# Kernel optimization log

Hardware: AMD Instinct MI355X
Metric: run time of the kernel (lower is better)

## Reference

```python
import jax, jax.numpy as jnp
import numpy as np

LN_EPS = 1e-5

def _layer_norm(x, g, b):
    mu = jnp.mean(x, axis=-1, keepdims=True)
    var = jnp.mean(jnp.square(x - mu), axis=-1, keepdims=True)
    return (x - mu) * jax.lax.rsqrt(var + LN_EPS) * g + b

def setup_inputs() -> dict:
    key = jax.random.key(0)
    ks = jax.random.split(key, 12)
    B, L, E, H, W = 4, 1024, 1024, 16, 128
    s = 0.02
    return {
        "x": jax.random.normal(ks[0], (B, L, E), dtype=jnp.float32),
        "in_proj_w": jax.random.normal(ks[1], (3 * E, E), dtype=jnp.float32) * s,
        "in_proj_b": jnp.zeros((3 * E,), dtype=jnp.float32),
        "out_proj_w": jax.random.normal(ks[2], (E, E), dtype=jnp.float32) * s,
        "out_proj_b": jnp.zeros((E,), dtype=jnp.float32),
        "ln1_g": jnp.ones((E,), dtype=jnp.float32),
        "ln1_b": jnp.zeros((E,), dtype=jnp.float32),
        "w1": jax.random.normal(ks[3], (4 * E, E), dtype=jnp.float32) * s,
        "b1": jnp.zeros((4 * E,), dtype=jnp.float32),
        "w2": jax.random.normal(ks[4], (E, 4 * E), dtype=jnp.float32) * s,
        "b2": jnp.zeros((E,), dtype=jnp.float32),
        "ln2_g": jnp.ones((E,), dtype=jnp.float32),
        "ln2_b": jnp.zeros((E,), dtype=jnp.float32),
        "n_head": 16,
        "window_size": 128,
    }

def reference(x, in_proj_w, in_proj_b, out_proj_w, out_proj_b,
              ln1_g, ln1_b, w1, b1, w2, b2, ln2_g, ln2_b,
              n_head, window_size):
    B, L, E = x.shape
    H = n_head
    D = E // H
    # qkv projection (torch Linear convention: y = x @ W.T + b)
    qkv = jnp.einsum('ble,fe->blf', x, in_proj_w) + in_proj_b  # [B,L,3E]
    q, k, v = jnp.split(qkv, 3, axis=-1)
    q = q.reshape(B, L, H, D).transpose(0, 2, 1, 3)  # [B,H,L,D]
    k = k.reshape(B, L, H, D).transpose(0, 2, 1, 3)
    v = v.reshape(B, L, H, D).transpose(0, 2, 1, 3)
    scores = jnp.einsum('bhld,bhmd->bhlm', q, k) / np.sqrt(D)  # [B,H,L,L]
    # banded window mask: allowed iff |i-j| <= window_size (same as the double loop)
    idx = jnp.arange(L)
    band = jnp.abs(idx[:, None] - idx[None, :]) <= window_size  # [L,L]
    scores = jnp.where(band[None, None], scores, -jnp.inf)
    attn = jax.nn.softmax(scores, axis=-1)  # [B,H,L,L]
    ctx = jnp.einsum('bhlm,bhmd->bhld', attn, v)  # [B,H,L,D]
    ctx = ctx.transpose(0, 2, 1, 3).reshape(B, L, E)
    attn_out = jnp.einsum('ble,fe->blf', ctx, out_proj_w) + out_proj_b
    attn_weights = jnp.mean(attn, axis=1)  # torch MHA averages heads -> [B,L,L]
    # residual + norm1 (dropout is identity in eval)
    h = _layer_norm(x + attn_out, ln1_g, ln1_b)
    # positionwise FFN
    ff = jnp.einsum('ble,fe->blf', h, w1) + b1
    ff = jax.nn.relu(ff)
    ff = jnp.einsum('blf,ef->ble', ff, w2) + b2
    out = _layer_norm(h + ff, ln2_g, ln2_b)
    return (out, attn_weights)
```

## Files before the change

kernel.cpp:

```cpp
#include <hip/hip_runtime.h>

#define BB 4
#define LL 1024
#define EE 1024
#define HH 16
#define DD 64

typedef __attribute__((ext_vector_type(8))) short short8;
typedef __attribute__((ext_vector_type(4))) float floatx4;

#define PSTR ((size_t)4096 * 1024)

__device__ __forceinline__ float bf2f(short s) {
    union { unsigned u; float f; } c;
    c.u = ((unsigned)(unsigned short)s) << 16;
    return c.f;
}
__device__ __forceinline__ short f2bf(float f) {
    union { float f; unsigned u; } c; c.f = f;
    unsigned r = c.u + 0x7fffu + ((c.u >> 16) & 1u);
    return (short)(r >> 16);
}

__device__ __forceinline__ void async_copy16(const void* g, void* l) {
    __builtin_amdgcn_global_load_lds(
        (const __attribute__((address_space(1))) unsigned int*)g,
        (__attribute__((address_space(3))) unsigned int*)l, 16, 0, 0);
}

__global__ __launch_bounds__(256) void cvt5(
    const float* __restrict__ x, const float* __restrict__ wqkv,
    const float* __restrict__ wo, const float* __restrict__ w1,
    const float* __restrict__ w2,
    short* __restrict__ xb, short* __restrict__ wqkvb, short* __restrict__ wob,
    short* __restrict__ w1b, short* __restrict__ w2b)
{
    int bi = blockIdx.x;
    const float* in; short* out; int base;
    if      (bi <  4096) { in = x;    out = xb;    base = 0;     }
    else if (bi <  7168) { in = wqkv; out = wqkvb; base = 4096;  }
    else if (bi <  8192) { in = wo;   out = wob;   base = 7168;  }
    else if (bi < 12288) { in = w1;   out = w1b;   base = 8192;  }
    else                 { in = w2;   out = w2b;   base = 12288; }
    int i = (bi - base) * 256 + threadIdx.x;
    float4 v = ((const float4*)in)[i];
    unsigned long long u =
          (unsigned long long)(unsigned short)f2bf(v.x)
        | ((unsigned long long)(unsigned short)f2bf(v.y) << 16)
        | ((unsigned long long)(unsigned short)f2bf(v.z) << 32)
        | ((unsigned long long)(unsigned short)f2bf(v.w) << 48);
    ((unsigned long long*)out)[i] = u;
}

template<bool RELU, bool SK, bool WVT>
__global__ __launch_bounds__(512, 2) void gemm256(
    const short* __restrict__ A, const short* __restrict__ Bw,
    const float* __restrict__ bias,
    short* __restrict__ Cb, short* __restrict__ VTp,
    int M, int N, int K, int Ksp)
{
    __shared__ short SH[67584];
    const int tid  = threadIdx.x;
    const int w    = tid >> 6, lane = tid & 63;
    const int fr   = lane & 15, quad = lane >> 4;
    const int wm   = w >> 2,  wn   = w & 3;

    const int gx   = gridDim.x;
    const int flat = blockIdx.y * gx + blockIdx.x;
    const int nwg  = gx * gridDim.y;
    const int q8   = nwg >> 3;
    const int swz  = (flat & 7) * q8 + (flat >> 3);
    const int m0   = (swz % gx) * 256;
    const int n0   = (swz / gx) * 256;

    const int kb = SK ? blockIdx.z * Ksp : 0;
    const int NT = (SK ? Ksp : K) >> 6;

    const int srow = w * 8 + (lane >> 3);
    const int sg   = lane & 7;
    auto stage = [&](int s) {
        if (s >= NT) return;
#pragma unroll
        for (int i = 0; i < 4; ++i) {
            int r = i * 64 + srow;
            int g = sg ^ (r & 7);
            async_copy16(A + (size_t)(m0 + r) * K + kb + s * 64 + g * 8,
                         SH + (s & 1) * 32768 + i * 4096 + w * 512);
        }
#pragma unroll
        for (int i = 0; i < 4; ++i) {
            int r = i * 64 + srow;
            int g = sg ^ (r & 7);
            async_copy16(Bw + (size_t)(n0 + r) * K + kb + s * 64 + g * 8,
                         SH + (s & 1) * 32768 + 16384 + i * 4096 + w * 512);
        }
    };

    floatx4 acc[8][4];
#pragma unroll
    for (int i = 0; i < 8; ++i)
#pragma unroll
        for (int j = 0; j < 4; ++j) acc[i][j] = (floatx4){0.f, 0.f, 0.f, 0.f};

    stage(0);

    const int posk0 = ((quad    ) ^ (fr & 7)) * 8;
    const int posk1 = ((4 + quad) ^ (fr & 7)) * 8;

    for (int t = 0; t < NT; ++t) {
        __syncthreads();
        __builtin_amdgcn_sched_barrier(0);

        const short* sA = SH + (t & 1) * 32768;
        const short* sB = sA + 16384;

        stage(t + 1);

        short8 a0[8], b0[4];
#pragma unroll
        for (int i = 0; i < 8; ++i) a0[i] = *(const short8*)&sA[(wm * 128 + i * 16 + fr) * 64 + posk0];
#pragma unroll
        for (int j = 0; j < 4; ++j) b0[j] = *(const short8*)&sB[(wn * 64 + j * 16 + fr) * 64 + posk0];
        __builtin_amdgcn_s_setprio(1);
#pragma unroll
        for (int i = 0; i < 8; ++i)
#pragma unroll
            for (int j = 0; j < 4; ++j)
                acc[i][j] = __builtin_amdgcn_mfma_f32_16x16x32_bf16(a0[i], b0[j], acc[i][j], 0, 0, 0);
        __builtin_amdgcn_s_setprio(0);

        short8 a1[8], b1[4];
#pragma unroll
        for (int i = 0; i < 8; ++i) a1[i] = *(const short8*)&sA[(wm * 128 + i * 16 + fr) * 64 + posk1];
#pragma unroll
        for (int j = 0; j < 4; ++j) b1[j] = *(const short8*)&sB[(wn * 64 + j * 16 + fr) * 64 + posk1];
        __builtin_amdgcn_s_setprio(1);
#pragma unroll
        for (int i = 0; i < 8; ++i)
#pragma unroll
            for (int j = 0; j < 4; ++j)
                acc[i][j] = __builtin_amdgcn_mfma_f32_16x16x32_bf16(a1[i], b1[j], acc[i][j], 0, 0, 0);
        __builtin_amdgcn_s_setprio(0);
    }

    __syncthreads();

    const int cc = lane & 15, rb4 = quad * 4;
    const bool vblk = WVT && (n0 >= 2048);

    if (!vblk) {
#pragma unroll
        for (int i = 0; i < 8; ++i) {
            int row = wm * 128 + i * 16 + rb4;
#pragma unroll
            for (int j = 0; j < 4; ++j) {
                int col = wn * 64 + j * 16 + cc;
                float bv = SK ? 0.0f : bias[n0 + col];
#pragma unroll
                for (int r = 0; r < 4; ++r) {
                    float v = acc[i][j][r] + bv;
                    if (RELU) v = fmaxf(v, 0.0f);
                    SH[(row + r) * 264 + col] = f2bf(v);
                }
            }
        }
    } else {
#pragma unroll
        for (int i = 0; i < 8; ++i) {
            int row = wm * 128 + i * 16 + rb4;
#pragma unroll
            for (int j = 0; j < 4; ++j) {
                int col = wn * 64 + j * 16 + cc;
                float bv = bias[n0 + col];
#pragma unroll
                for (int r = 0; r < 4; ++r)
                    SH[col * 264 + row + r] = f2bf(acc[i][j][r] + bv);
            }
        }
    }
    __syncthreads();

    if (!vblk) {
        short* Co = Cb + (SK ? (size_t)blockIdx.z * PSTR : 0);
#pragma unroll
        for (int it = 0; it < 16; ++it) {
            int idx = it * 512 + tid;
            int row = idx >> 5, ch = idx & 31;
            short8 v = *(const short8*)&SH[row * 264 + ch * 8];
            *(short8*)&Co[(size_t)(m0 + row) * N + n0 + ch * 8] = v;
        }
    } else {
        const int bI = m0 >> 10, m0l = m0 & 1023;
#pragma unroll
        for (int it = 0; it < 16; ++it) {
            int idx = it * 512 + tid;
            int col = idx >> 5, tc = idx & 31;
            int gc  = n0 + col - 2048;
            int h   = gc >> 6, d = gc & 63;
            short8 v = *(const short8*)&SH[col * 264 + tc * 8];
            *(short8*)&VTp[((size_t)((bI * 16 + h) * 64 + d)) * 1024 + m0l + tc * 8] = v;
        }
    }
}

template<bool RELU, bool SK>
__global__ __launch_bounds__(256) void gemm_bt(
    const short* __restrict__ A, const short* __restrict__ Bw,
    const float* __restrict__ bias,
    short* __restrict__ Cb,
    int M, int N, int K, int Ksp)
{
    __shared__ union U {
        struct { short As[128 * 64]; short Bs[128 * 64]; } s;
        short Cs[128 * 136];
    } u;
    const int tid  = threadIdx.x;
    const int wave = tid >> 6, lane = tid & 63;
    const int m0 = blockIdx.x * 128, n0 = blockIdx.y * 128;
    const int wm = (wave & 1) * 64, wn = (wave >> 1) * 64;
    const int kbase = SK ? blockIdx.z * Ksp : 0;

    floatx4 acc[4][4];
#pragma unroll
    for (int i = 0; i < 4; ++i)
#pragma unroll
        for (int j = 0; j < 4; ++j) acc[i][j] = (floatx4){0.f, 0.f, 0.f, 0.f};

    const int srow = wave * 8 + (lane >> 3);
    const int scol = (((lane & 7) ^ ((lane >> 3) & 7))) * 8;
    const short* gA = A  + (size_t)(m0 + srow) * K + kbase + scol;
    const short* gB = Bw + (size_t)(n0 + srow) * K + kbase + scol;
    short* lA = u.s.As + wave * 512;
    short* lB = u.s.Bs + wave * 512;

    const int fr = lane & 15, quad = lane >> 4;
    const int kiters = (SK ? Ksp : K) >> 6;
    for (int kt = 0; kt < kiters; ++kt) {
#pragma unroll
        for (int s = 0; s < 4; ++s) {
            async_copy16(gA + (size_t)s * 32 * K, lA + s * 2048);
            async_copy16(gB + (size_t)s * 32 * K, lB + s * 2048);
        }
        gA += 64; gB += 64;
        __syncthreads();
#pragma unroll
        for (int ks = 0; ks < 2; ++ks) {
            short8 af[4], bf[4];
#pragma unroll
            for (int i = 0; i < 4; ++i) {
                int pos = ((ks * 4 + quad) ^ (fr & 7)) * 8;
                af[i] = *(const short8*)&u.s.As[(wm + i * 16 + fr) * 64 + pos];
                bf[i] = *(const short8*)&u.s.Bs[(wn + i * 16 + fr) * 64 + pos];
            }
#pragma unroll
            for (int i = 0; i < 4; ++i)
#pragma unroll
                for (int j = 0; j < 4; ++j)
                    acc[i][j] = __builtin_amdgcn_mfma_f32_16x16x32_bf16(af[i], bf[j], acc[i][j], 0, 0, 0);
        }
        __syncthreads();
    }

    const int cc = lane & 15;
    const int rb = (lane >> 4) * 4;
#pragma unroll
    for (int j = 0; j < 4; ++j) {
        int col = wn + j * 16 + cc;
        float bv = SK ? 0.0f : bias[n0 + col];
#pragma unroll
        for (int i = 0; i < 4; ++i) {
            int row = wm + i * 16 + rb;
#pragma unroll
            for (int r = 0; r < 4; ++r) {
                float v = acc[i][j][r] + bv;
                if (RELU) v = fmaxf(v, 0.0f);
                u.Cs[(row + r) * 136 + col] = f2bf(v);
            }
        }
    }
    __syncthreads();
    short* Co = Cb + (SK ? (size_t)blockIdx.z * PSTR : 0);
    const int trow = tid >> 4, tcol = (tid & 15) * 8;
#pragma unroll
    for (int p = 0; p < 8; ++p) {
        int row = p * 16 + trow;
        short8 vv = *(const short8*)&u.Cs[row * 136 + tcol];
        *(short8*)&Co[(size_t)(m0 + row) * N + n0 + tcol] = vv;
    }
}

__global__ __launch_bounds__(256) void ln_kernel(
    const float* __restrict__ xa, const short* __restrict__ parts, int nparts,
    const float* __restrict__ bias,
    const float* __restrict__ g, const float* __restrict__ beta,
    float* __restrict__ outf, short* __restrict__ outb)
{
    const int row = blockIdx.x;
    const int tid = threadIdx.x;
    float4 va = ((const float4*)(xa + (size_t)row * EE))[tid];
    float4 vb = ((const float4*)bias)[tid];
    float v0 = va.x + vb.x, v1 = va.y + vb.y, v2 = va.z + vb.z, v3 = va.w + vb.w;
#pragma unroll 4
    for (int p = 0; p < nparts; ++p) {
        unsigned long long u8 = ((const unsigned long long*)(parts + p * PSTR + (size_t)row * EE))[tid];
        v0 += bf2f((short)(u8 & 0xffff));
        v1 += bf2f((short)((u8 >> 16) & 0xffff));
        v2 += bf2f((short)((u8 >> 32) & 0xffff));
        v3 += bf2f((short)(u8 >> 48));
    }
    float s  = v0 + v1 + v2 + v3;
    float ss = v0 * v0 + v1 * v1 + v2 * v2 + v3 * v3;
#pragma unroll
    for (int o = 1; o < 64; o <<= 1) { s += __shfl_xor(s, o); ss += __shfl_xor(ss, o); }
    __shared__ float red[8];
    if ((tid & 63) == 0) { red[(tid >> 6) * 2] = s; red[(tid >> 6) * 2 + 1] = ss; }
    __syncthreads();
    s  = red[0] + red[2] + red[4] + red[6];
    ss = red[1] + red[3] + red[5] + red[7];
    float mean = s * (1.0f / EE);
    float var  = ss * (1.0f / EE) - mean * mean;
    float rstd = rsqrtf(var + 1e-5f);
    float4 vg = ((const float4*)g)[tid];
    float4 vt = ((const float4*)beta)[tid];
    float o0 = (v0 - mean) * rstd * vg.x + vt.x;
    float o1 = (v1 - mean) * rstd * vg.y + vt.y;
    float o2 = (v2 - mean) * rstd * vg.z + vt.z;
    float o3 = (v3 - mean) * rstd * vg.w + vt.w;
    if (outf) ((float4*)(outf + (size_t)row * EE))[tid] = make_float4(o0, o1, o2, o3);
    if (outb) {
        unsigned long long u =
              (unsigned long long)(unsigned short)f2bf(o0)
            | ((unsigned long long)(unsigned short)f2bf(o1) << 16)
            | ((unsigned long long)(unsigned short)f2bf(o2) << 32)
            | ((unsigned long long)(unsigned short)f2bf(o3) << 48);
        ((unsigned long long*)(outb + (size_t)row * EE))[tid] = u;
    }
}

__global__ __launch_bounds__(512, 6) void attn_mfma(
    const short* __restrict__ qkv,
    const short* __restrict__ vt,
    short* __restrict__ ctxp,
    short* __restrict__ pb)
{
    __shared__ short Kl[64 * 320];
    __shared__ float Red[2][2][64];
    const int tid = threadIdx.x, w = tid >> 6, lane = tid & 63;
    const int quad = lane >> 4, mcol = lane & 15;
    const int id = blockIdx.x;
    const int i0 = (id >> 6) * 64, h = id & 15, b = (id >> 4) & 3;
    const int jb0 = i0 - 128;

    const short* qb = qkv + (size_t)(b * 1024) * 3072 + h * 64;
    const short* kb = qb + 1024;

    {
        short* dstb = Kl + w * 512;
#pragma unroll
        for (int it = 0; it < 5; ++it) {
            int jo = it * 64 + w * 8 + (lane >> 3);
            int j  = min(max(jb0 + jo, 0), 1023);
            int g  = (lane & 7) ^ (jo & 7);
            async_copy16(kb + (size_t)j * 3072 + g * 8, dstb + it * 4096);
        }
    }

    const int mt = w >> 1, qtr = w & 1;
    const short* qrow = qb + (size_t)(i0 + mt * 16 + mcol) * 3072 + quad * 8;
    short8 aq0 = *(const short8*)qrow;
    short8 aq1 = *(const short8*)(qrow + 32);

    __syncthreads();

    floatx4 sacc[10];
#pragma unroll
    for (int c = 0; c < 10; ++c) sacc[c] = (floatx4){0.f, 0.f, 0.f, 0.f};
#pragma unroll
    for (int c = 0; c < 10; ++c) {
        int jo = qtr * 160 + c * 16 + mcol;
        const short* krow = Kl + jo * 64;
        short8 b0 = *(const short8*)&krow[((quad    ) ^ (jo & 7)) * 8];
        short8 b1 = *(const short8*)&krow[((4 + quad) ^ (jo & 7)) * 8];
        sacc[c] = __builtin_amdgcn_mfma_f32_16x16x32_bf16(aq0, b0, sacc[c], 0, 0, 0);
        sacc[c] = __builtin_amdgcn_mfma_f32_16x16x32_bf16(aq1, b1, sacc[c], 0, 0, 0);
    }

    const int row0 = mt * 16 + quad * 4;
#pragma unroll
    for (int r = 0; r < 4; ++r) {
        int row = row0 + r;
        float m = -1e30f;
#pragma unroll
        for (int c = 0; c < 10; ++c) {
            int jo = qtr * 160 + c * 16 + mcol;
            bool val = (jo >= row) && (jo <= row + 256) && ((unsigned)(jb0 + jo) < 1024u);
            float s = val ? sacc[c][r] * 0.125f : -1e30f;
            sacc[c][r] = s;
            m = fmaxf(m, s);
        }
        m = fmaxf(m, __shfl_xor(m, 1));
        m = fmaxf(m, __shfl_xor(m, 2));
        m = fmaxf(m, __shfl_xor(m, 4));
        m = fmaxf(m, __shfl_xor(m, 8));
        if (mcol == 0) Red[qtr][0][row] = m;
    }
    __syncthreads();
#pragma unroll
    for (int r = 0; r < 4; ++r) {
        int row = row0 + r;
        float M = fmaxf(Red[0][0][row], Red[1][0][row]);
        float l = 0.f;
#pragma unroll
        for (int c = 0; c < 10; ++c) {
            float p = __expf(sacc[c][r] - M);
            sacc[c][r] = p;
            l += p;
        }
        l += __shfl_xor(l, 1);
        l += __shfl_xor(l, 2);
        l += __shfl_xor(l, 4);
        l += __shfl_xor(l, 8);
        if (mcol == 0) Red[qtr][1][row] = l;
    }
    __syncthreads();
    short* Pl = Kl;
#pragma unroll
    for (int r = 0; r < 4; ++r) {
        int row = row0 + r;
        float inv = 1.0f / (Red[0][1][row] + Red[1][1][row]);
#pragma unroll
        for (int c = 0; c < 10; ++c) {
            int jo = qtr * 160 + c * 16 + mcol;
            Pl[row * 320 + (((jo >> 3) ^ (row & 7)) * 8) + (jo & 7)] = f2bf(sacc[c][r] * inv);
        }
    }
    __syncthreads();

    const int pmt = w & 3, dth = w >> 2;
    floatx4 cacc[2];
    cacc[0] = (floatx4){0.f, 0.f, 0.f, 0.f};
    cacc[1] = (floatx4){0.f, 0.f, 0.f, 0.f};
    const int prow = (pmt * 16 + mcol) * 320;
    const short* vb0 = vt + ((size_t)((b * 16 + h) * 64 + dth * 32) + mcol) * 1024;
#pragma unroll
    for (int jc = 0; jc < 10; ++jc) {
        short8 ap = *(const short8*)&Pl[prow + (((jc * 4 + quad) ^ (mcol & 7)) * 8)];
        int jg = jb0 + jc * 32 + quad * 8;
        if ((unsigned)jg >= 1024u) jg = 0;
        short8 bv0 = *(const short8*)(vb0 + jg);
        short8 bv1 = *(const short8*)(vb0 + (size_t)16 * 1024 + jg);
        cacc[0] = __builtin_amdgcn_mfma_f32_16x16x32_bf16(ap, bv0, cacc[0], 0, 0, 0);
        cacc[1] = __builtin_amdgcn_mfma_f32_16x16x32_bf16(ap, bv1, cacc[1], 0, 0, 0);
    }

    short* pbb = pb + ((size_t)((b * 16 + h) * 1024) + i0) * 320;
#pragma unroll
    for (int s = 0; s < 5; ++s) {
        int t = s * 512 + tid;
        int row = t / 40, c = t - row * 40;
        short8 v = *(const short8*)&Pl[row * 320 + ((c ^ (row & 7)) * 8)];
        *(short8*)&pbb[(size_t)t * 8] = v;
    }
    __syncthreads();

    short* Ct = Kl;
#pragma unroll
    for (int d2 = 0; d2 < 2; ++d2)
#pragma unroll
        for (int r = 0; r < 4; ++r)
            Ct[(pmt * 16 + quad * 4 + r) * 72 + dth * 32 + d2 * 16 + mcol] = f2bf(cacc[d2][r]);
    __syncthreads();
    short* cb = ctxp + (size_t)(b * 1024 + i0) * 1024 + h * 64;
    {
        int row = tid >> 3, c = tid & 7;
        short8 v = *(const short8*)&Ct[row * 72 + c * 8];
        *(short8*)&cb[(size_t)row * 1024 + c * 8] = v;
    }
}

__global__ __launch_bounds__(256) void pb_reduce(const short* __restrict__ pb,
                                                 float* __restrict__ aw)
{
    const int i = blockIdx.x & 1023, b = blockIdx.x >> 10;
    const int i0 = i & ~63;
    __shared__ short P[16 * 320];
    for (int t = threadIdx.x; t < 640; t += 256) {
        int hh = t / 40, c = t - hh * 40;
        ((short8*)P)[t] = *(const short8*)(pb +
            ((size_t)((b * 16 + hh) * 1024) + i) * 320 + c * 8);
    }
    __syncthreads();
    float* row = aw + ((size_t)(b * 1024) + i) * 1024;
    for (int j = threadIdx.x; j < 1024; j += 256) {
        int jo = j - i0 + 128;
        float s = 0.f;
        if ((unsigned)jo < 320u) {
#pragma unroll
            for (int hh = 0; hh < 16; ++hh)
                s += bf2f(P[hh * 320 + jo]);
            s *= (1.0f / 16.0f);
        }
        row[j] = s;
    }
}

extern "C" void kernel_launch(void* const* d_in, const int* in_sizes, int n_in,
                              void* d_out, int out_size, void* d_ws, size_t ws_size,
                              hipStream_t stream) {
    const float* x    = (const float*)d_in[0];
    const float* wqkv = (const float*)d_in[1];
    const float* bqkv = (const float*)d_in[2];
    const float* wo   = (const float*)d_in[3];
    const float* bo   = (const float*)d_in[4];
    const float* g1   = (const float*)d_in[5];
    const float* be1  = (const float*)d_in[6];
    const float* w1   = (const float*)d_in[7];
    const float* bb1  = (const float*)d_in[8];
    const float* w2   = (const float*)d_in[9];
    const float* bb2  = (const float*)d_in[10];
    const float* g2   = (const float*)d_in[11];
    const float* be2  = (const float*)d_in[12];

    char* ws = (char*)d_ws;
    size_t off = 0;
    auto take = [&](size_t bytes) {
        void* p = ws + off;
        off += (bytes + 255) & ~(size_t)255;
        return p;
    };
    short* xb     = (short*)take((size_t)4096 * 1024 * 2);
    short* wqkv_b = (short*)take((size_t)3072 * 1024 * 2);
    short* wo_b   = (short*)take((size_t)1024 * 1024 * 2);
    short* w1_b   = (short*)take((size_t)4096 * 1024 * 2);
    short* w2_b   = (short*)take((size_t)1024 * 4096 * 2);
    short* qkv_b  = (short*)take((size_t)4096 * 3072 * 2);
    short* ctx_b  = (short*)take((size_t)4096 * 1024 * 2);
    short* ff2_p  = qkv_b;
    short* attn_p = (short*)take((size_t)2 * 4096 * 1024 * 2);
    float* h_f    = (float*)take((size_t)4096 * 1024 * 4);
    short* vt_ws  = (short*)h_f;
    short* h_b    = (short*)take((size_t)4096 * 1024 * 2);
    short* pb_ws  = (short*)take((size_t)4 * 16 * 1024 * 320 * 2);
    short* ff_b   = pb_ws;

    float* out_f = (float*)d_out;
    float* attnW = (float*)d_out + (size_t)4 * 1024 * 1024;

    cvt5<<<16384, 256, 0, stream>>>(x, wqkv, wo, w1, w2, xb, wqkv_b, wo_b, w1_b, w2_b);

    gemm256<false, false, true><<<dim3(16, 12), 512, 0, stream>>>(
        xb, wqkv_b, bqkv, qkv_b, vt_ws, 4096, 3072, 1024, 1024);

    attn_mfma<<<1024, 512, 0, stream>>>(qkv_b, vt_ws, ctx_b, pb_ws);

    pb_reduce<<<4096, 256, 0, stream>>>(pb_ws, attnW);

    gemm_bt<false, true><<<dim3(32, 8, 2), 256, 0, stream>>>(
        ctx_b, wo_b, nullptr, attn_p, 4096, 1024, 1024, 512);

    ln_kernel<<<4096, 256, 0, stream>>>(x, attn_p, 2, bo, g1, be1, h_f, h_b);

    gemm256<true, false, false><<<dim3(16, 16), 512, 0, stream>>>(
        h_b, w1_b, bb1, ff_b, nullptr, 4096, 4096, 1024, 1024);

    gemm256<false, true, false><<<dim3(16, 4, 4), 512, 0, stream>>>(
        ff_b, w2_b, nullptr, ff2_p, nullptr, 4096, 1024, 4096, 1024);

    ln_kernel<<<4096, 256, 0, stream>>>(h_f, ff2_p, 4, bb2, g2, be2, out_f, nullptr);
}
```

Baseline: 320.9 us.

## Double-buffer out-projection GEMM LDS tiles and relax attention occupancy bound

```diff
diff --git a/kernel.cpp b/kernel.cpp
--- a/kernel.cpp
+++ b/kernel.cpp
@@ -203,22 +203,40 @@
     }
 }
 
-template<bool RELU, bool SK>
-__global__ __launch_bounds__(256) void gemm_bt(
+template<bool SK>
+__global__ __launch_bounds__(256, 2) void gemm_bt2(
     const short* __restrict__ A, const short* __restrict__ Bw,
-    const float* __restrict__ bias,
     short* __restrict__ Cb,
     int M, int N, int K, int Ksp)
 {
-    __shared__ union U {
-        struct { short As[128 * 64]; short Bs[128 * 64]; } s;
-        short Cs[128 * 136];
-    } u;
+    __shared__ short SH[32768];
     const int tid  = threadIdx.x;
-    const int wave = tid >> 6, lane = tid & 63;
+    const int w    = tid >> 6, lane = tid & 63;
+    const int fr   = lane & 15, quad = lane >> 4;
+    const int wm   = w >> 1, wn = w & 1;
     const int m0 = blockIdx.x * 128, n0 = blockIdx.y * 128;
-    const int wm = (wave & 1) * 64, wn = (wave >> 1) * 64;
-    const int kbase = SK ? blockIdx.z * Ksp : 0;
+    const int kb = SK ? blockIdx.z * Ksp : 0;
+    const int NT = (SK ? Ksp : K) >> 6;
+
+    const int sr8 = tid >> 3;
+    const int sg  = tid & 7;
+    auto stage = [&](int s) {
+        if (s >= NT) return;
+#pragma unroll
+        for (int i = 0; i < 4; ++i) {
+            int r = i * 32 + sr8;
+            int g = sg ^ (r & 7);
+            async_copy16(A + (size_t)(m0 + r) * K + kb + s * 64 + g * 8,
+                         SH + (s & 1) * 16384 + i * 2048 + w * 512);
+        }
+#pragma unroll
+        for (int i = 0; i < 4; ++i) {
+            int r = i * 32 + sr8;
+            int g = sg ^ (r & 7);
+            async_copy16(Bw + (size_t)(n0 + r) * K + kb + s * 64 + g * 8,
+                         SH + (s & 1) * 16384 + 8192 + i * 2048 + w * 512);
+        }
+    };
 
     floatx4 acc[4][4];
 #pragma unroll
@@ -226,56 +244,59 @@
 #pragma unroll
         for (int j = 0; j < 4; ++j) acc[i][j] = (floatx4){0.f, 0.f, 0.f, 0.f};
 
-    const int srow = wave * 8 + (lane >> 3);
-    const int scol = (((lane & 7) ^ ((lane >> 3) & 7))) * 8;
-    const short* gA = A  + (size_t)(m0 + srow) * K + kbase + scol;
-    const short* gB = Bw + (size_t)(n0 + srow) * K + kbase + scol;
-    short* lA = u.s.As + wave * 512;
-    short* lB = u.s.Bs + wave * 512;
-
-    const int fr = lane & 15, quad = lane >> 4;
-    const int kiters = (SK ? Ksp : K) >> 6;
-    for (int kt = 0; kt < kiters; ++kt) {
-#pragma unroll
-        for (int s = 0; s < 4; ++s) {
-            async_copy16(gA + (size_t)s * 32 * K, lA + s * 2048);
-            async_copy16(gB + (size_t)s * 32 * K, lB + s * 2048);
-        }
-        gA += 64; gB += 64;
+    stage(0);
+
+    const int posk0 = ((quad    ) ^ (fr & 7)) * 8;
+    const int posk1 = ((4 + quad) ^ (fr & 7)) * 8;
+
+    for (int t = 0; t < NT; ++t) {
         __syncthreads();
-#pragma unroll
-        for (int ks = 0; ks < 2; ++ks) {
-            short8 af[4], bf[4];
-#pragma unroll
-            for (int i = 0; i < 4; ++i) {
-                int pos = ((ks * 4 + quad) ^ (fr & 7)) * 8;
-                af[i] = *(const short8*)&u.s.As[(wm + i * 16 + fr) * 64 + pos];
-                bf[i] = *(const short8*)&u.s.Bs[(wn + i * 16 + fr) * 64 + pos];
-            }
-#pragma unroll
-            for (int i = 0; i < 4; ++i)
-#pragma unroll
-                for (int j = 0; j < 4; ++j)
-                    acc[i][j] = __builtin_amdgcn_mfma_f32_16x16x32_bf16(af[i], bf[j], acc[i][j], 0, 0, 0);
-        }
-        __syncthreads();
-    }
-
-    const int cc = lane & 15;
-    const int rb = (lane >> 4) * 4;
-#pragma unroll
-    for (int j = 0; j < 4; ++j) {
-        int col = wn + j * 16 + cc;
-        float bv = SK ? 0.0f : bias[n0 + col];
-#pragma unroll
-        for (int i = 0; i < 4; ++i) {
-            int row = wm + i * 16 + rb;
-#pragma unroll
-            for (int r = 0; r < 4; ++r) {
-                float v = acc[i][j][r] + bv;
-                if (RELU) v = fmaxf(v, 0.0f);
-                u.Cs[(row + r) * 136 + col] = f2bf(v);
-            }
+        __builtin_amdgcn_sched_barrier(0);
+
+        const short* sA = SH + (t & 1) * 16384;
+        const short* sB = sA + 8192;
+
+        stage(t + 1);
+
+        short8 a0[4], b0[4];
+#pragma unroll
+        for (int i = 0; i < 4; ++i) a0[i] = *(const short8*)&sA[(wm * 64 + i * 16 + fr) * 64 + posk0];
+#pragma unroll
+        for (int j = 0; j < 4; ++j) b0[j] = *(const short8*)&sB[(wn * 64 + j * 16 + fr) * 64 + posk0];
+        __builtin_amdgcn_s_setprio(1);
+#pragma unroll
+        for (int i = 0; i < 4; ++i)
+#pragma unroll
+            for (int j = 0; j < 4; ++j)
+                acc[i][j] = __builtin_amdgcn_mfma_f32_16x16x32_bf16(a0[i], b0[j], acc[i][j], 0, 0, 0);
+        __builtin_amdgcn_s_setprio(0);
+
+        short8 a1[4], b1[4];
+#pragma unroll
+        for (int i = 0; i < 4; ++i) a1[i] = *(const short8*)&sA[(wm * 64 + i * 16 + fr) * 64 + posk1];
+#pragma unroll
+        for (int j = 0; j < 4; ++j) b1[j] = *(const short8*)&sB[(wn * 64 + j * 16 + fr) * 64 + posk1];
+        __builtin_amdgcn_s_setprio(1);
+#pragma unroll
+        for (int i = 0; i < 4; ++i)
+#pragma unroll
+            for (int j = 0; j < 4; ++j)
+                acc[i][j] = __builtin_amdgcn_mfma_f32_16x16x32_bf16(a1[i], b1[j], acc[i][j], 0, 0, 0);
+        __builtin_amdgcn_s_setprio(0);
+    }
+
+    __syncthreads();
+
+    const int cc = lane & 15, rb4 = quad * 4;
+#pragma unroll
+    for (int i = 0; i < 4; ++i) {
+        int row = wm * 64 + i * 16 + rb4;
+#pragma unroll
+        for (int j = 0; j < 4; ++j) {
+            int col = wn * 64 + j * 16 + cc;
+#pragma unroll
+            for (int r = 0; r < 4; ++r)
+                SH[(row + r) * 136 + col] = f2bf(acc[i][j][r]);
         }
     }
     __syncthreads();
@@ -284,7 +305,7 @@
 #pragma unroll
     for (int p = 0; p < 8; ++p) {
         int row = p * 16 + trow;
-        short8 vv = *(const short8*)&u.Cs[row * 136 + tcol];
+        short8 vv = *(const short8*)&SH[row * 136 + tcol];
         *(short8*)&Co[(size_t)(m0 + row) * N + n0 + tcol] = vv;
     }
 }
@@ -337,7 +358,7 @@
     }
 }
 
-__global__ __launch_bounds__(512, 6) void attn_mfma(
+__global__ __launch_bounds__(512, 4) void attn_mfma(
     const short* __restrict__ qkv,
     const short* __restrict__ vt,
     short* __restrict__ ctxp,
@@ -555,8 +576,8 @@
 
     pb_reduce<<<4096, 256, 0, stream>>>(pb_ws, attnW);
 
-    gemm_bt<false, true><<<dim3(32, 8, 2), 256, 0, stream>>>(
-        ctx_b, wo_b, nullptr, attn_p, 4096, 1024, 1024, 512);
+    gemm_bt2<true><<<dim3(32, 8, 2), 256, 0, stream>>>(
+        ctx_b, wo_b, attn_p, 4096, 1024, 1024, 512);
 
     ln_kernel<<<4096, 256, 0, stream>>>(x, attn_p, 2, bo, g1, be1, h_f, h_b);
 
```

Result: no change. 321.0 us, median of 2 (+0.0%).
